# Performance work log

Hardware: AMD Instinct MI355X
Metric: run time of the kernel (lower is better)

## Reference

```python
import jax, jax.numpy as jnp
import numpy as np

NUM_HEADS = 16
LN_EPS = 1e-5


def _rope(x):
    """lucidrains RotaryEmbedding(dim_per_head // 2): rotate only the first
    Dh//2 channels with interleaved pairs; pass the rest through.
    x: (B, H, S, Dh)"""
    S, D = x.shape[-2], x.shape[-1]
    rot = D // 2
    inv_freq = 1.0 / (10000.0 ** (jnp.arange(0, rot, 2, dtype=jnp.float32) / rot))  # (rot//2,)
    ang = jnp.arange(S, dtype=jnp.float32)[:, None] * inv_freq[None, :]             # (S, rot//2)
    ang = jnp.repeat(ang, 2, axis=-1)                                               # (S, rot)
    cos, sin = jnp.cos(ang), jnp.sin(ang)
    xr, xp = x[..., :rot], x[..., rot:]
    x1, x2 = xr[..., 0::2], xr[..., 1::2]
    rot_half = jnp.stack((-x2, x1), axis=-1).reshape(xr.shape)  # interleaved (-x2, x1)
    xr = xr * cos + rot_half * sin
    return jnp.concatenate([xr, xp], axis=-1)


def setup_inputs() -> dict:
    key = jax.random.key(0)
    k1, k2, k3 = jax.random.split(key, 3)
    B, S, D = 4, 2048, 2048
    X = jax.random.normal(k1, (B, S, D), dtype=jnp.float32)
    ln_w = jnp.ones((D,), dtype=jnp.float32)
    ln_b = jnp.zeros((D,), dtype=jnp.float32)
    W_in = jax.random.normal(k2, (D, 3 * D), dtype=jnp.float32) * 0.02
    W_out = jax.random.normal(k3, (D, D), dtype=jnp.float32) * 0.02
    return {"X": X, "ln_w": ln_w, "ln_b": ln_b, "W_in": W_in, "W_out": W_out}


def reference(X, ln_w, ln_b, W_in, W_out):
    B, S, D = X.shape
    H = NUM_HEADS
    Dh = D // H
    # pre-norm (LayerNorm)
    mu = jnp.mean(X, axis=-1, keepdims=True)
    var = jnp.mean(jnp.square(X - mu), axis=-1, keepdims=True)
    Xn = (X - mu) * jax.lax.rsqrt(var + LN_EPS) * ln_w + ln_b
    # fused QKV projection
    qkv = jnp.einsum('bsd,df->bsf', Xn, W_in)            # (B, S, 3D)
    Q, K, V = jnp.split(qkv, 3, axis=-1)
    Q = Q.reshape(B, S, H, Dh).transpose(0, 2, 1, 3)     # (B, H, S, Dh)
    K = K.reshape(B, S, H, Dh).transpose(0, 2, 1, 3)
    V = V.reshape(B, S, H, Dh).transpose(0, 2, 1, 3)
    Q, K = _rope(Q), _rope(K)
    scores = jnp.einsum('bhqd,bhkd->bhqk', Q, K) / jnp.sqrt(jnp.float32(Dh))
    probs = jax.nn.softmax(scores, axis=-1)              # acausal: no mask
    ctx = jnp.einsum('bhqk,bhkd->bhqd', probs, V)
    ctx = ctx.transpose(0, 2, 1, 3).reshape(B, S, D)
    out = jnp.einsum('bsd,df->bsf', ctx, W_out)
    return out + X
```

## Files before the change

### kernel.cpp

```cpp
#include <hip/hip_runtime.h>
#include <hip/hip_bf16.h>
#include <cstddef>

#define B_ 4
#define S_ 2048
#define D_ 2048
#define H_ 16
#define DH_ 128
#define F_ 6144
#define BS_ 8192

typedef __attribute__((ext_vector_type(8))) short bfrag8;
typedef __attribute__((ext_vector_type(4))) float ffrag4;

typedef const __attribute__((address_space(1))) void* gptr1;
typedef __attribute__((address_space(3))) void* lptr3;
#define GL16(g, l) __builtin_amdgcn_global_load_lds((gptr1)(g), (lptr3)(l), 16, 0, 0)

__device__ __forceinline__ short f2bf(float f) {
  unsigned u = __float_as_uint(f);
  u = (u + 0x7FFFu + ((u >> 16) & 1u)) >> 16;
  return (short)u;
}
__device__ __forceinline__ float bf2f(short s) {
  return __uint_as_float(((unsigned)(unsigned short)s) << 16);
}
__device__ __forceinline__ unsigned pk2(float lo, float hi) {
  unsigned a = __float_as_uint(lo);
  a = (a + 0x7FFFu + ((a >> 16) & 1u)) >> 16;
  unsigned b = __float_as_uint(hi);
  b = (b + 0x7FFFu + ((b >> 16) & 1u)) & 0xFFFF0000u;
  return a | b;
}

__global__ __launch_bounds__(256) void ln_kernel(const float* __restrict__ X,
    const float* __restrict__ w, const float* __restrict__ bta,
    short* __restrict__ Xn) {
  int row = blockIdx.x;
  int tid = threadIdx.x;
  const float* xr = X + (size_t)row * D_;
  float x[8];
  float4 v0 = *(const float4*)(xr + tid * 4);
  float4 v1 = *(const float4*)(xr + 1024 + tid * 4);
  x[0] = v0.x; x[1] = v0.y; x[2] = v0.z; x[3] = v0.w;
  x[4] = v1.x; x[5] = v1.y; x[6] = v1.z; x[7] = v1.w;
  float sum = 0.f, ssq = 0.f;
#pragma unroll
  for (int i = 0; i < 8; i++) { sum += x[i]; ssq += x[i] * x[i]; }
#pragma unroll
  for (int off = 1; off < 64; off <<= 1) {
    sum += __shfl_xor(sum, off, 64);
    ssq += __shfl_xor(ssq, off, 64);
  }
  __shared__ float s1[4], s2[4];
  int wave = tid >> 6;
  if ((tid & 63) == 0) { s1[wave] = sum; s2[wave] = ssq; }
  __syncthreads();
  sum = s1[0] + s1[1] + s1[2] + s1[3];
  ssq = s2[0] + s2[1] + s2[2] + s2[3];
  float mu = sum * (1.0f / D_);
  float var = ssq * (1.0f / D_) - mu * mu;
  float rs = rsqrtf(var + 1e-5f);
  short* orow = Xn + (size_t)row * D_;
#pragma unroll
  for (int i = 0; i < 8; i++) {
    int col = (i < 4) ? (tid * 4 + i) : (1024 + tid * 4 + (i - 4));
    float xn = (x[i] - mu) * rs * w[col] + bta[col];
    orow[col] = f2bf(xn);
  }
}

__global__ __launch_bounds__(256) void transpose_cvt(const float* __restrict__ W,
    short* __restrict__ WT, int R, int C) {
  __shared__ float t[32][33];
  int tx = threadIdx.x, ty = threadIdx.y;
  int c0 = blockIdx.x * 32, r0 = blockIdx.y * 32;
#pragma unroll
  for (int i = 0; i < 4; i++)
    t[ty + i * 8][tx] = W[(size_t)(r0 + ty + i * 8) * C + c0 + tx];
  __syncthreads();
#pragma unroll
  for (int i = 0; i < 4; i++)
    WT[(size_t)(c0 + ty + i * 8) * R + r0 + tx] = f2bf(t[tx][ty + i * 8]);
}

template<int EPI>
__global__ __launch_bounds__(256) void gemm_bt(const short* __restrict__ A,
    const short* __restrict__ Bt, short* __restrict__ Cb, float* __restrict__ Cf,
    const float* __restrict__ resid, int M, int N, int K) {
  __shared__ __align__(16) short lA[128 * 64];
  __shared__ __align__(16) short lB[128 * 64];
  int tid = threadIdx.x;
  int m0 = blockIdx.y * 128, n0 = blockIdx.x * 128;
  int wave = tid >> 6, lane = tid & 63;
  int m16 = lane & 15, quad = lane >> 4;
  int wm = (wave >> 1) * 64, wn = (wave & 1) * 64;
  const ffrag4 fzero = {0.f, 0.f, 0.f, 0.f};
  ffrag4 acc[4][4];
#pragma unroll
  for (int i = 0; i < 4; i++)
#pragma unroll
    for (int j = 0; j < 4; j++) acc[i][j] = fzero;

  int srow = (lane >> 3);
  int scb  = lane & 7;
  for (int k0 = 0; k0 < K; k0 += 64) {
#pragma unroll
    for (int i = 0; i < 4; i++) {
      int c = i * 4 + wave;
      int r = c * 8 + srow;
      int sb = scb ^ (r & 7);
      GL16(A + (size_t)(m0 + r) * K + k0 + sb * 8, lA + c * 512);
      GL16(Bt + (size_t)(n0 + r) * K + k0 + sb * 8, lB + c * 512);
    }
    __syncthreads();
#pragma unroll
    for (int kk = 0; kk < 2; kk++) {
      bfrag8 af[4], bfb[4];
#pragma unroll
      for (int t = 0; t < 4; t++) {
        int ra = wm + t * 16 + m16;
        int rb = wn + t * 16 + m16;
        int blk = (kk * 4 + quad);
        af[t] = *(const bfrag8*)(lA + ra * 64 + ((blk ^ (m16 & 7)) << 3));
        bfb[t] = *(const bfrag8*)(lB + rb * 64 + ((blk ^ (m16 & 7)) << 3));
      }
#pragma unroll
      for (int i = 0; i < 4; i++)
#pragma unroll
        for (int j = 0; j < 4; j++)
          acc[i][j] = __builtin_amdgcn_mfma_f32_16x16x32_bf16(af[i], bfb[j], acc[i][j], 0, 0, 0);
    }
    __syncthreads();
  }

#pragma unroll
  for (int i = 0; i < 4; i++) {
    int rowb = m0 + wm + i * 16 + quad * 4;
#pragma unroll
    for (int j = 0; j < 4; j++) {
      int col = n0 + wn + j * 16 + m16;
#pragma unroll
      for (int r = 0; r < 4; r++) {
        float v = acc[i][j][r];
        size_t idx = (size_t)(rowb + r) * N + col;
        if (EPI == 0) Cb[idx] = f2bf(v);
        else Cf[idx] = v + resid[idx];
      }
    }
  }
}

__global__ __launch_bounds__(256) void rope_kernel(short* __restrict__ qkv) {
  int idx = blockIdx.x * 256 + threadIdx.x;
  int j = idx & 31;
  int h = (idx >> 5) & 15;
  int which = (idx >> 9) & 1;
  int row = idx >> 10;
  int s = row & (S_ - 1);
  float invf = exp2f(-(float)j * (13.287712379549449f / 32.0f));
  float ang = (float)s * invf;
  float sn, cs;
  sincosf(ang, &sn, &cs);
  size_t base = (size_t)row * F_ + (size_t)which * D_ + h * DH_ + 2 * j;
  unsigned v = *(unsigned*)(qkv + base);
  float x1 = bf2f((short)(v & 0xFFFF));
  float x2 = bf2f((short)(v >> 16));
  float o1 = x1 * cs - x2 * sn;
  float o2 = x2 * cs + x1 * sn;
  unsigned ov = (unsigned)(unsigned short)f2bf(o1) |
                ((unsigned)(unsigned short)f2bf(o2) << 16);
  *(unsigned*)(qkv + base) = ov;
}

__global__ __launch_bounds__(256) void vtrans_kernel(const short* __restrict__ qkv,
    short* __restrict__ Vt) {
  __shared__ unsigned short t[32][33];
  int tx = threadIdx.x, ty = threadIdx.y;
  int s0 = blockIdx.x * 32;
  int d0 = blockIdx.y * 32;
  int bh = blockIdx.z;
  int b = bh >> 4, h = bh & 15;
#pragma unroll
  for (int i = 0; i < 4; i++)
    t[ty + i * 8][tx] =
      (unsigned short)qkv[(size_t)(b * S_ + s0 + ty + i * 8) * F_ + 2 * D_ + h * DH_ + d0 + tx];
  __syncthreads();
#pragma unroll
  for (int i = 0; i < 4; i++)
    Vt[(size_t)(bh * DH_ + d0 + ty + i * 8) * S_ + s0 + tx] = (short)t[tx][ty + i * 8];
}

__global__ __launch_bounds__(512) void attn_kernel(const short* __restrict__ qkv,
    const short* __restrict__ Vt, short* __restrict__ ctx) {
  __shared__ __align__(16) short lK[2][64 * 128];
  __shared__ __align__(16) short lV[2][128 * 64];
  int tid = threadIdx.x;
  int wave = tid >> 6, lane = tid & 63;
  int m16 = lane & 15, quad = lane >> 4;
  int bh = blockIdx.y;
  int b = bh >> 4, h = bh & 15;
  int qbase = blockIdx.x * 256 + wave * 32;

  const float qscale = 1.4426950408889634f * 0.08838834764831845f;
  bfrag8 qf[2][4];
#pragma unroll
  for (int qb = 0; qb < 2; qb++)
#pragma unroll
    for (int kc = 0; kc < 4; kc++) {
      bfrag8 q = *(const bfrag8*)(qkv +
          (size_t)(b * S_ + qbase + qb * 16 + m16) * F_ + h * DH_ + kc * 32 + quad * 8);
#pragma unroll
      for (int j = 0; j < 8; j++) q[j] = f2bf(bf2f(q[j]) * qscale);
      qf[qb][kc] = q;
    }

  const ffrag4 fzero = {0.f, 0.f, 0.f, 0.f};
  ffrag4 oacc[2][8];
#pragma unroll
  for (int qb = 0; qb < 2; qb++)
#pragma unroll
    for (int nd = 0; nd < 8; nd++) oacc[qb][nd] = fzero;
  float lpart[2] = {0.f, 0.f};

  int krow = lane >> 4;
  int kcb = lane & 15;
  int vrow = lane >> 3;
  int vcb = lane & 7;

  {
    int sk0 = 0;
#pragma unroll
    for (int i = 0; i < 2; i++) {
      int c = wave + i * 8;
      int r = c * 4 + krow;
      int sb = kcb ^ (r & 15);
      GL16(qkv + (size_t)(b * S_ + sk0 + r) * F_ + D_ + h * DH_ + sb * 8, &lK[0][c * 512]);
    }
#pragma unroll
    for (int i = 0; i < 2; i++) {
      int c = wave + i * 8;
      int r = c * 8 + vrow;
      int sb = vcb ^ (r & 7);
      GL16(Vt + (size_t)(bh * DH_ + r) * S_ + sk0 + sb * 8, &lV[0][c * 512]);
    }
  }
  __syncthreads();

  for (int kt = 0; kt < 32; kt++) {
    int cur = kt & 1;
    if (kt < 31) {
      int sk0 = (kt + 1) * 64;
      int nb = cur ^ 1;
#pragma unroll
      for (int i = 0; i < 2; i++) {
        int c = wave + i * 8;
        int r = c * 4 + krow;
        int sb = kcb ^ (r & 15);
        GL16(qkv + (size_t)(b * S_ + sk0 + r) * F_ + D_ + h * DH_ + sb * 8, &lK[nb][c * 512]);
      }
#pragma unroll
      for (int i = 0; i < 2; i++) {
        int c = wave + i * 8;
        int r = c * 8 + vrow;
        int sb = vcb ^ (r & 7);
        GL16(Vt + (size_t)(bh * DH_ + r) * S_ + sk0 + sb * 8, &lV[nb][c * 512]);
      }
    }

    const short* kb = &lK[cur][0];
    const short* vb = &lV[cur][0];

    ffrag4 sacc[2][4];
#pragma unroll
    for (int qb = 0; qb < 2; qb++)
#pragma unroll
      for (int ntk = 0; ntk < 4; ntk++) sacc[qb][ntk] = fzero;
#pragma unroll
    for (int ntk = 0; ntk < 4; ntk++)
#pragma unroll
      for (int kc = 0; kc < 4; kc++) {
        bfrag8 kf = *(const bfrag8*)(kb + (ntk * 16 + m16) * 128 +
                                     (((kc * 4 + quad) ^ m16) << 3));
        sacc[0][ntk] = __builtin_amdgcn_mfma_f32_16x16x32_bf16(kf, qf[0][kc], sacc[0][ntk], 0, 0, 0);
        sacc[1][ntk] = __builtin_amdgcn_mfma_f32_16x16x32_bf16(kf, qf[1][kc], sacc[1][ntk], 0, 0, 0);
      }

    bfrag8 pA[2][2];
#pragma unroll
    for (int qb = 0; qb < 2; qb++) {
      unsigned Xp[4][2];
      float ls = 0.f;
#pragma unroll
      for (int ntk = 0; ntk < 4; ntk++) {
        float e0 = exp2f(sacc[qb][ntk][0]);
        float e1 = exp2f(sacc[qb][ntk][1]);
        float e2 = exp2f(sacc[qb][ntk][2]);
        float e3 = exp2f(sacc[qb][ntk][3]);
        ls += (e0 + e1) + (e2 + e3);
        Xp[ntk][0] = pk2(e0, e1);
        Xp[ntk][1] = pk2(e2, e3);
      }
      lpart[qb] += ls;
#pragma unroll
      for (int kc = 0; kc < 2; kc++) {
        unsigned x0 = Xp[2 * kc][0], x1 = Xp[2 * kc][1];
        unsigned y0 = Xp[2 * kc + 1][0], y1 = Xp[2 * kc + 1][1];
        asm("v_permlane32_swap_b32 %0, %1" : "+v"(x0), "+v"(y0));
        asm("v_permlane16_swap_b32 %0, %1" : "+v"(x0), "+v"(y0));
        asm("v_permlane32_swap_b32 %0, %1" : "+v"(x1), "+v"(y1));
        asm("v_permlane16_swap_b32 %0, %1" : "+v"(x1), "+v"(y1));
        union { int4 i4; bfrag8 b8; } u;
        u.i4 = (int4){(int)x0, (int)x1, (int)y0, (int)y1};
        pA[qb][kc] = u.b8;
      }
    }

#pragma unroll
    for (int kc = 0; kc < 2; kc++)
#pragma unroll
      for (int nd = 0; nd < 8; nd++) {
        bfrag8 vf = *(const bfrag8*)(vb + (nd * 16 + m16) * 64 +
                                     (((kc * 4 + quad) ^ (m16 & 7)) << 3));
        oacc[0][nd] = __builtin_amdgcn_mfma_f32_16x16x32_bf16(pA[0][kc], vf, oacc[0][nd], 0, 0, 0);
        oacc[1][nd] = __builtin_amdgcn_mfma_f32_16x16x32_bf16(pA[1][kc], vf, oacc[1][nd], 0, 0, 0);
      }

    __syncthreads();
  }

#pragma unroll
  for (int qb = 0; qb < 2; qb++) {
    lpart[qb] += __shfl_xor(lpart[qb], 16, 64);
    lpart[qb] += __shfl_xor(lpart[qb], 32, 64);
  }
#pragma unroll
  for (int qb = 0; qb < 2; qb++) {
    float inv[4];
#pragma unroll
    for (int r = 0; r < 4; r++) inv[r] = 1.0f / __shfl(lpart[qb], quad * 4 + r, 64);
#pragma unroll
    for (int nd = 0; nd < 8; nd++)
#pragma unroll
      for (int r = 0; r < 4; r++) {
        int row = qbase + qb * 16 + quad * 4 + r;
        int col = h * DH_ + nd * 16 + m16;
        ctx[(size_t)(b * S_ + row) * D_ + col] = f2bf(oacc[qb][nd][r] * inv[r]);
      }
  }
}

extern "C" void kernel_launch(void* const* d_in, const int* in_sizes, int n_in,
                              void* d_out, int out_size, void* d_ws, size_t ws_size,
                              hipStream_t stream) {
  const float* X    = (const float*)d_in[0];
  const float* lnw  = (const float*)d_in[1];
  const float* lnb  = (const float*)d_in[2];
  const float* Win  = (const float*)d_in[3];
  const float* Wout = (const float*)d_in[4];
  float* out = (float*)d_out;
  char* ws = (char*)d_ws;
  short* Xn    = (short*)(ws + 0);
  short* WinT  = (short*)(ws + 33554432);
  short* WoutT = (short*)(ws + 58720256);
  short* qkv   = (short*)(ws + 67108864);
  short* Vt    = (short*)(ws + 167772160);
  short* ctx   = (short*)(ws + 201326592);

  transpose_cvt<<<dim3(192, 64), dim3(32, 8), 0, stream>>>(Win, WinT, 2048, 6144);
  transpose_cvt<<<dim3(64, 64), dim3(32, 8), 0, stream>>>(Wout, WoutT, 2048, 2048);
  ln_kernel<<<8192, 256, 0, stream>>>(X, lnw, lnb, Xn);
  gemm_bt<0><<<dim3(48, 64), 256, 0, stream>>>(Xn, WinT, qkv, nullptr, nullptr, 8192, 6144, 2048);
  rope_kernel<<<32768, 256, 0, stream>>>(qkv);
  vtrans_kernel<<<dim3(64, 4, 64), dim3(32, 8), 0, stream>>>(qkv, Vt);
  attn_kernel<<<dim3(8, 64), 512, 0, stream>>>(qkv, Vt, ctx);
  gemm_bt<1><<<dim3(16, 64), 256, 0, stream>>>(ctx, WoutT, nullptr, out, X, 8192, 2048, 2048);
}
```

Baseline: 727.1 us.

## Fuse RoPE and V transpose into QKV GEMM epilogue, enlarge GEMM M-tile

The QKV GEMM epilogue now applies rotary embedding to the rotated Q/K channels, using a lane shuffle to fetch each pair partner, and writes V directly in transposed layout. This removes the separate rope and V-transpose kernels and their extra passes over the QKV buffer, and the QK buffer shrinks to 4096 columns. Both GEMMs also move to a 256x128 tile with launch_bounds(256,2), doubling per-wave accumulators for more operand reuse. The cost is higher register pressure, lower occupancy, fewer blocks, and scattered short4 stores for V.

```diff
diff --git a/kernel.cpp b/kernel.cpp
--- a/kernel.cpp
+++ b/kernel.cpp
@@ -7,7 +7,7 @@
 #define D_ 2048
 #define H_ 16
 #define DH_ 128
-#define F_ 6144
+#define QKS_ 4096
 #define BS_ 8192
 
 typedef __attribute__((ext_vector_type(8))) short bfrag8;
@@ -85,48 +85,56 @@
 }
 
 template<int EPI>
-__global__ __launch_bounds__(256) void gemm_bt(const short* __restrict__ A,
-    const short* __restrict__ Bt, short* __restrict__ Cb, float* __restrict__ Cf,
-    const float* __restrict__ resid, int M, int N, int K) {
-  __shared__ __align__(16) short lA[128 * 64];
+__global__ __launch_bounds__(256, 2) void gemm_bt(const short* __restrict__ A,
+    const short* __restrict__ Bt, short* __restrict__ Cb, short* __restrict__ Vt,
+    float* __restrict__ Cf, const float* __restrict__ resid, int M, int N, int K) {
+  __shared__ __align__(16) short lA[256 * 64];
   __shared__ __align__(16) short lB[128 * 64];
   int tid = threadIdx.x;
-  int m0 = blockIdx.y * 128, n0 = blockIdx.x * 128;
+  int m0 = blockIdx.y * 256, n0 = blockIdx.x * 128;
   int wave = tid >> 6, lane = tid & 63;
   int m16 = lane & 15, quad = lane >> 4;
-  int wm = (wave >> 1) * 64, wn = (wave & 1) * 64;
+  int wm = (wave >> 1) * 128, wn = (wave & 1) * 64;
   const ffrag4 fzero = {0.f, 0.f, 0.f, 0.f};
-  ffrag4 acc[4][4];
-#pragma unroll
-  for (int i = 0; i < 4; i++)
+  ffrag4 acc[8][4];
+#pragma unroll
+  for (int i = 0; i < 8; i++)
 #pragma unroll
     for (int j = 0; j < 4; j++) acc[i][j] = fzero;
 
-  int srow = (lane >> 3);
+  int srow = lane >> 3;
   int scb  = lane & 7;
   for (int k0 = 0; k0 < K; k0 += 64) {
 #pragma unroll
-    for (int i = 0; i < 4; i++) {
-      int c = i * 4 + wave;
+    for (int i = 0; i < 8; i++) {
+      int c = wave * 8 + i;
       int r = c * 8 + srow;
       int sb = scb ^ (r & 7);
       GL16(A + (size_t)(m0 + r) * K + k0 + sb * 8, lA + c * 512);
+    }
+#pragma unroll
+    for (int i = 0; i < 4; i++) {
+      int c = wave * 4 + i;
+      int r = c * 8 + srow;
+      int sb = scb ^ (r & 7);
       GL16(Bt + (size_t)(n0 + r) * K + k0 + sb * 8, lB + c * 512);
     }
     __syncthreads();
 #pragma unroll
     for (int kk = 0; kk < 2; kk++) {
-      bfrag8 af[4], bfb[4];
+      bfrag8 af[8], bfb[4];
+#pragma unroll
+      for (int t = 0; t < 8; t++) {
+        int ra = wm + t * 16 + m16;
+        af[t] = *(const bfrag8*)(lA + ra * 64 + (((kk * 4 + quad) ^ (ra & 7)) << 3));
+      }
 #pragma unroll
       for (int t = 0; t < 4; t++) {
-        int ra = wm + t * 16 + m16;
         int rb = wn + t * 16 + m16;
-        int blk = (kk * 4 + quad);
-        af[t] = *(const bfrag8*)(lA + ra * 64 + ((blk ^ (m16 & 7)) << 3));
-        bfb[t] = *(const bfrag8*)(lB + rb * 64 + ((blk ^ (m16 & 7)) << 3));
-      }
-#pragma unroll
-      for (int i = 0; i < 4; i++)
+        bfb[t] = *(const bfrag8*)(lB + rb * 64 + (((kk * 4 + quad) ^ (rb & 7)) << 3));
+      }
+#pragma unroll
+      for (int i = 0; i < 8; i++)
 #pragma unroll
         for (int j = 0; j < 4; j++)
           acc[i][j] = __builtin_amdgcn_mfma_f32_16x16x32_bf16(af[i], bfb[j], acc[i][j], 0, 0, 0);
@@ -135,60 +143,45 @@
   }
 
 #pragma unroll
-  for (int i = 0; i < 4; i++) {
+  for (int i = 0; i < 8; i++) {
     int rowb = m0 + wm + i * 16 + quad * 4;
 #pragma unroll
     for (int j = 0; j < 4; j++) {
       int col = n0 + wn + j * 16 + m16;
-#pragma unroll
-      for (int r = 0; r < 4; r++) {
-        float v = acc[i][j][r];
-        size_t idx = (size_t)(rowb + r) * N + col;
-        if (EPI == 0) Cb[idx] = f2bf(v);
-        else Cf[idx] = v + resid[idx];
-      }
-    }
-  }
-}
-
-__global__ __launch_bounds__(256) void rope_kernel(short* __restrict__ qkv) {
-  int idx = blockIdx.x * 256 + threadIdx.x;
-  int j = idx & 31;
-  int h = (idx >> 5) & 15;
-  int which = (idx >> 9) & 1;
-  int row = idx >> 10;
-  int s = row & (S_ - 1);
-  float invf = exp2f(-(float)j * (13.287712379549449f / 32.0f));
-  float ang = (float)s * invf;
-  float sn, cs;
-  sincosf(ang, &sn, &cs);
-  size_t base = (size_t)row * F_ + (size_t)which * D_ + h * DH_ + 2 * j;
-  unsigned v = *(unsigned*)(qkv + base);
-  float x1 = bf2f((short)(v & 0xFFFF));
-  float x2 = bf2f((short)(v >> 16));
-  float o1 = x1 * cs - x2 * sn;
-  float o2 = x2 * cs + x1 * sn;
-  unsigned ov = (unsigned)(unsigned short)f2bf(o1) |
-                ((unsigned)(unsigned short)f2bf(o2) << 16);
-  *(unsigned*)(qkv + base) = ov;
-}
-
-__global__ __launch_bounds__(256) void vtrans_kernel(const short* __restrict__ qkv,
-    short* __restrict__ Vt) {
-  __shared__ unsigned short t[32][33];
-  int tx = threadIdx.x, ty = threadIdx.y;
-  int s0 = blockIdx.x * 32;
-  int d0 = blockIdx.y * 32;
-  int bh = blockIdx.z;
-  int b = bh >> 4, h = bh & 15;
-#pragma unroll
-  for (int i = 0; i < 4; i++)
-    t[ty + i * 8][tx] =
-      (unsigned short)qkv[(size_t)(b * S_ + s0 + ty + i * 8) * F_ + 2 * D_ + h * DH_ + d0 + tx];
-  __syncthreads();
-#pragma unroll
-  for (int i = 0; i < 4; i++)
-    Vt[(size_t)(bh * DH_ + d0 + ty + i * 8) * S_ + s0 + tx] = (short)t[tx][ty + i * 8];
+      if (EPI == 1) {
+#pragma unroll
+        for (int r = 0; r < 4; r++) {
+          size_t idx = (size_t)(rowb + r) * N + col;
+          Cf[idx] = acc[i][j][r] + resid[idx];
+        }
+      } else if (col >= 4096) {
+        int d = col - 4096;
+        short4 pk;
+        pk.x = f2bf(acc[i][j][0]);
+        pk.y = f2bf(acc[i][j][1]);
+        pk.z = f2bf(acc[i][j][2]);
+        pk.w = f2bf(acc[i][j][3]);
+        *(short4*)(Vt + ((size_t)((rowb >> 11) * H_ + (d >> 7)) * DH_ + (d & 127)) * S_ +
+                   (rowb & (S_ - 1))) = pk;
+      } else if ((col & 127) < 64) {
+        int p = (col & 127) >> 1;
+        float invf = exp2f(-(float)p * (13.287712379549449f / 32.0f));
+        float sgn = (col & 1) ? 1.0f : -1.0f;
+#pragma unroll
+        for (int r = 0; r < 4; r++) {
+          float own = acc[i][j][r];
+          float prt = __shfl_xor(own, 1, 64);
+          float sn, cs;
+          sincosf((float)((rowb + r) & (S_ - 1)) * invf, &sn, &cs);
+          Cb[(size_t)(rowb + r) * QKS_ + col] = f2bf(own * cs + sgn * prt * sn);
+        }
+      } else {
+#pragma unroll
+        for (int r = 0; r < 4; r++)
+          Cb[(size_t)(rowb + r) * QKS_ + col] = f2bf(acc[i][j][r]);
+      }
+    }
+  }
 }
 
 __global__ __launch_bounds__(512) void attn_kernel(const short* __restrict__ qkv,
@@ -209,7 +202,7 @@
 #pragma unroll
     for (int kc = 0; kc < 4; kc++) {
       bfrag8 q = *(const bfrag8*)(qkv +
-          (size_t)(b * S_ + qbase + qb * 16 + m16) * F_ + h * DH_ + kc * 32 + quad * 8);
+          (size_t)(b * S_ + qbase + qb * 16 + m16) * QKS_ + h * DH_ + kc * 32 + quad * 8);
 #pragma unroll
       for (int j = 0; j < 8; j++) q[j] = f2bf(bf2f(q[j]) * qscale);
       qf[qb][kc] = q;
@@ -229,20 +222,19 @@
   int vcb = lane & 7;
 
   {
-    int sk0 = 0;
 #pragma unroll
     for (int i = 0; i < 2; i++) {
       int c = wave + i * 8;
       int r = c * 4 + krow;
       int sb = kcb ^ (r & 15);
-      GL16(qkv + (size_t)(b * S_ + sk0 + r) * F_ + D_ + h * DH_ + sb * 8, &lK[0][c * 512]);
+      GL16(qkv + (size_t)(b * S_ + r) * QKS_ + D_ + h * DH_ + sb * 8, &lK[0][c * 512]);
     }
 #pragma unroll
     for (int i = 0; i < 2; i++) {
       int c = wave + i * 8;
       int r = c * 8 + vrow;
       int sb = vcb ^ (r & 7);
-      GL16(Vt + (size_t)(bh * DH_ + r) * S_ + sk0 + sb * 8, &lV[0][c * 512]);
+      GL16(Vt + (size_t)(bh * DH_ + r) * S_ + sb * 8, &lV[0][c * 512]);
     }
   }
   __syncthreads();
@@ -257,7 +249,7 @@
         int c = wave + i * 8;
         int r = c * 4 + krow;
         int sb = kcb ^ (r & 15);
-        GL16(qkv + (size_t)(b * S_ + sk0 + r) * F_ + D_ + h * DH_ + sb * 8, &lK[nb][c * 512]);
+        GL16(qkv + (size_t)(b * S_ + sk0 + r) * QKS_ + D_ + h * DH_ + sb * 8, &lK[nb][c * 512]);
       }
 #pragma unroll
       for (int i = 0; i < 2; i++) {
@@ -364,15 +356,13 @@
   short* WinT  = (short*)(ws + 33554432);
   short* WoutT = (short*)(ws + 58720256);
   short* qkv   = (short*)(ws + 67108864);
-  short* Vt    = (short*)(ws + 167772160);
-  short* ctx   = (short*)(ws + 201326592);
+  short* Vt    = (short*)(ws + 134217728);
+  short* ctx   = (short*)(ws + 167772160);
 
   transpose_cvt<<<dim3(192, 64), dim3(32, 8), 0, stream>>>(Win, WinT, 2048, 6144);
   transpose_cvt<<<dim3(64, 64), dim3(32, 8), 0, stream>>>(Wout, WoutT, 2048, 2048);
   ln_kernel<<<8192, 256, 0, stream>>>(X, lnw, lnb, Xn);
-  gemm_bt<0><<<dim3(48, 64), 256, 0, stream>>>(Xn, WinT, qkv, nullptr, nullptr, 8192, 6144, 2048);
-  rope_kernel<<<32768, 256, 0, stream>>>(qkv);
-  vtrans_kernel<<<dim3(64, 4, 64), dim3(32, 8), 0, stream>>>(qkv, Vt);
+  gemm_bt<0><<<dim3(48, 32), 256, 0, stream>>>(Xn, WinT, qkv, Vt, nullptr, nullptr, 8192, 6144, 2048);
   attn_kernel<<<dim3(8, 64), 512, 0, stream>>>(qkv, Vt, ctx);
-  gemm_bt<1><<<dim3(16, 64), 256, 0, stream>>>(ctx, WoutT, nullptr, out, X, 8192, 2048, 2048);
-}
+  gemm_bt<1><<<dim3(16, 32), 256, 0, stream>>>(ctx, WoutT, nullptr, nullptr, out, X, 8192, 2048, 2048);
+}
```

Result: slower. 1.592 ms (+118.9%).
